# Kernel tuning notes

Measured on AMD Instinct MI355X. Metric: run time of the kernel, lower is better.

## Reference

```python
import jax, jax.numpy as jnp
import numpy as np

INPUT_SZ = 512
HIDDEN_SZ = 512
BATCH = 64
SEQ = 512


def setup_inputs() -> dict:
    key = jax.random.key(0)
    k_x, k_ih, k_hh = jax.random.split(key, 3)
    x = jax.random.normal(k_x, (BATCH, SEQ, INPUT_SZ), dtype=jnp.float32)
    # xavier-uniform style init for 2-D params, zeros for bias (as in init_weights)
    lim_ih = float(np.sqrt(6.0 / (INPUT_SZ + 4 * HIDDEN_SZ)))
    lim_hh = float(np.sqrt(6.0 / (HIDDEN_SZ + 4 * HIDDEN_SZ)))
    weight_ih = jax.random.uniform(k_ih, (INPUT_SZ, 4 * HIDDEN_SZ), jnp.float32, -lim_ih, lim_ih)
    weight_hh = jax.random.uniform(k_hh, (HIDDEN_SZ, 4 * HIDDEN_SZ), jnp.float32, -lim_hh, lim_hh)
    bias = jnp.zeros((4 * HIDDEN_SZ,), jnp.float32)
    h0 = jnp.zeros((1, BATCH, HIDDEN_SZ), jnp.float32)
    c0 = jnp.zeros((1, BATCH, HIDDEN_SZ), jnp.float32)
    return {"x": x, "weight_ih": weight_ih, "weight_hh": weight_hh, "bias": bias, "h0": h0, "c0": c0}


def reference(x, weight_ih, weight_hh, bias, h0, c0):
    HS = weight_hh.shape[0]
    # Precompute input projection for all timesteps: (seq, batch, 4*HS)
    x_proj = jnp.einsum('bsi,ih->sbh', x, weight_ih)

    def step(carry, xp_t):
        h_t, c_t = carry  # (1, b, HS)
        gates = xp_t[None] + h_t @ weight_hh + bias  # (1, b, 4*HS)
        i_t = jax.nn.sigmoid(gates[..., :HS])
        f_t = jax.nn.sigmoid(gates[..., HS:2 * HS])
        g_t = jnp.tanh(gates[..., 2 * HS:3 * HS])
        o_t = jax.nn.sigmoid(gates[..., 3 * HS:])
        c_t = f_t * c_t + i_t * g_t
        h_t = o_t * jnp.tanh(c_t)
        return (h_t, c_t), h_t[0]  # emit (b, HS)

    (h_T, c_T), hs = jax.lax.scan(step, (h0, c0), x_proj)
    hidden_seq = jnp.transpose(hs, (1, 0, 2))  # (batch, seq, HS)
    return hidden_seq, h_T, c_T
```

## Files before the change

### kernel.cpp

```cpp
#include <hip/hip_runtime.h>

#define SEQ   512
#define BATCH 64
#define IS    512
#define HS    512
#define G4    2048

typedef _Float16 half8 __attribute__((ext_vector_type(8)));
typedef _Float16 half4 __attribute__((ext_vector_type(4)));
typedef float floatx4 __attribute__((ext_vector_type(4)));
typedef unsigned long long ull;

__device__ __forceinline__ float sigm(float x) {
    return 1.0f / (1.0f + __expf(-x));
}
__device__ __forceinline__ float tanh_(float x) {
    float e = __expf(-2.0f * fabsf(x));
    float r = (1.0f - e) / (1.0f + e);
    return copysignf(r, x);
}

__global__ void convert_f32_f16(const float* __restrict__ in,
                                _Float16* __restrict__ out, int n4) {
    int i = blockIdx.x * blockDim.x + threadIdx.x;
    if (i < n4) {
        float4 v = ((const float4*)in)[i];
        half4 o = { (_Float16)v.x, (_Float16)v.y, (_Float16)v.z, (_Float16)v.w };
        ((half4*)out)[i] = o;
    }
}

__global__ void transpose_w(const float* __restrict__ in, _Float16* __restrict__ out) {
    __shared__ _Float16 tile[64][72];
    int bk = blockIdx.x & 7;
    int bn = blockIdx.x >> 3;
    int c = threadIdx.x & 63;
    int r4 = threadIdx.x >> 6;
    #pragma unroll
    for (int rr = 0; rr < 16; rr++) {
        int k = rr * 4 + r4;
        tile[k][c] = (_Float16)in[(size_t)(bk * 64 + k) * 2048 + bn * 64 + c];
    }
    __syncthreads();
    #pragma unroll
    for (int rr = 0; rr < 16; rr++) {
        int n = rr * 4 + r4;
        out[(size_t)(bn * 64 + n) * 512 + bk * 64 + c] = tile[c][n];
    }
}

__global__ void __launch_bounds__(256, 2) gemm_xproj(
    const _Float16* __restrict__ A,
    const _Float16* __restrict__ Bt,
    _Float16* __restrict__ xp) {
    __shared__ _Float16 As[4096];
    __shared__ _Float16 Bs[4096];
    const int tid = threadIdx.x;
    const int w = tid >> 6, l = tid & 63, lr = l & 15, q = l >> 4;
    const int bm = blockIdx.x & 255, bn = blockIdx.x >> 8;
    const int row0 = bm * 128, col0 = bn * 128;
    const int wr = (w >> 1) * 64, wc = (w & 1) * 64;

    floatx4 zz = {0.f, 0.f, 0.f, 0.f};
    floatx4 acc[4][4];
    #pragma unroll
    for (int mt = 0; mt < 4; mt++)
        #pragma unroll
        for (int ct = 0; ct < 4; ct++) acc[mt][ct] = zz;

    for (int kt = 0; kt < 16; kt++) {
        __syncthreads();
        #pragma unroll
        for (int rnd = 0; rnd < 2; rnd++) {
            int o = tid * 16 + rnd * 4096;
            int r = o >> 6;
            int ke = (o & 63) >> 1;
            *(half8*)((char*)As + o) = *(const half8*)(A  + (size_t)(row0 + r) * 512 + kt * 32 + ke);
            *(half8*)((char*)Bs + o) = *(const half8*)(Bt + (size_t)(col0 + r) * 512 + kt * 32 + ke);
        }
        __syncthreads();
        half8 af[4], bf[4];
        #pragma unroll
        for (int mt = 0; mt < 4; mt++)
            af[mt] = *(const half8*)(As + (wr + mt * 16 + lr) * 32 + q * 8);
        #pragma unroll
        for (int ct = 0; ct < 4; ct++)
            bf[ct] = *(const half8*)(Bs + (wc + ct * 16 + lr) * 32 + q * 8);
        #pragma unroll
        for (int mt = 0; mt < 4; mt++)
            #pragma unroll
            for (int ct = 0; ct < 4; ct++)
                acc[mt][ct] = __builtin_amdgcn_mfma_f32_16x16x32_f16(af[mt], bf[ct], acc[mt][ct], 0, 0, 0);
    }
    #pragma unroll
    for (int mt = 0; mt < 4; mt++) {
        #pragma unroll
        for (int r = 0; r < 4; r++) {
            int row = row0 + wr + mt * 16 + q * 4 + r;
            int t = row & 511, b = row >> 9;
            #pragma unroll
            for (int ct = 0; ct < 4; ct++) {
                int col = col0 + wc + ct * 16 + lr;
                int hid = col & 511, gate = col >> 9;
                int wgd = (b >> 4) * 32 + (hid >> 4);
                int bl = b & 15, u = hid & 15;
                xp[(size_t)(((t * 128 + wgd) * 16 + bl)) * 64 + u * 4 + gate] =
                    (_Float16)acc[mt][ct][r];
            }
        }
    }
}

__global__ void __launch_bounds__(64, 1) lstm_scan(
    const _Float16* __restrict__ xp,
    const _Float16* __restrict__ wt,
    _Float16* __restrict__ hb,
    const float* __restrict__ bias,
    const float* __restrict__ h0,
    const float* __restrict__ c0,
    float* __restrict__ out,
    int* __restrict__ ep) {
    __shared__ _Float16 wlds[16384];
    __shared__ _Float16 scr[320];
    const int wg = blockIdx.x;
    const int bg = wg >> 5;
    const int hg = wg & 31;
    const int l  = threadIdx.x;
    const int lr = l & 15;
    const int q  = l >> 4;
    const int myhid = hg * 16 + lr;

    for (int idx = l; idx < 2048; idx += 64) {
        int n = idx >> 6, g = idx & 63;
        int gate = n >> 4, u = n & 15;
        half8 v = *(const half8*)(wt + (size_t)(gate * 512 + hg * 16 + u) * 512 + g * 8);
        *(half8*)(wlds + n * 512 + ((g ^ (n & 7)) * 8)) = v;
    }
    half8 wreg[16][2];
    #pragma unroll
    for (int kt = 0; kt < 16; kt++)
        #pragma unroll
        for (int gg = 0; gg < 2; gg++)
            wreg[kt][gg] = *(const half8*)(wt + (size_t)((2 + gg) * 512 + hg * 16 + lr) * 512 + kt * 32 + q * 8);

    {
        int b = l >> 2, u4 = (l & 3) * 4;
        union { _Float16 h[4]; ull u; } pk;
        #pragma unroll
        for (int k2 = 0; k2 < 4; k2++)
            pk.h[k2] = (_Float16)h0[(bg * 16 + b) * 512 + hg * 16 + u4 + k2];
        __hip_atomic_store((ull*)hb + bg * 2048 + b * 128 + hg * 4 + (l & 3), pk.u,
                           __ATOMIC_RELAXED, __HIP_MEMORY_SCOPE_AGENT);
    }

    float bs[4], c[4];
    #pragma unroll
    for (int g4 = 0; g4 < 4; g4++) bs[g4] = bias[g4 * 512 + myhid];
    #pragma unroll
    for (int r = 0; r < 4; r++) c[r] = c0[(bg * 16 + q * 4 + r) * 512 + myhid];

    half4 xv[4];
    #pragma unroll
    for (int r = 0; r < 4; r++)
        xv[r] = *(const half4*)(xp + (((size_t)0 * 128 + wg) * 16 + q * 4 + r) * 64 + lr * 4);

    asm volatile("s_waitcnt vmcnt(0)" ::: "memory");
    if (l == 0)
        __hip_atomic_store(&ep[bg * 32 + hg], 1,
                           __ATOMIC_RELAXED, __HIP_MEMORY_SCOPE_AGENT);

    int* const eline = &ep[bg * 32 + (l & 31)];

    for (int t = 0; t < 512; t++) {
        const int tgt = t + 1;
        while (!__all(__hip_atomic_load(eline, __ATOMIC_RELAXED,
                                        __HIP_MEMORY_SCOPE_AGENT) >= tgt)) { }
        asm volatile("" ::: "memory");
        __builtin_amdgcn_sched_barrier(0);

        const ull* hsrc = (const ull*)hb + (size_t)((t & 1) * 4 + bg) * 2048;
        union HU { ull u[2]; half8 v; } a[16];
        #pragma unroll
        for (int kt = 0; kt < 16; kt++) {
            int idx = lr * 128 + kt * 8 + q * 2;
            a[kt].u[0] = __hip_atomic_load(hsrc + idx,     __ATOMIC_RELAXED, __HIP_MEMORY_SCOPE_AGENT);
            a[kt].u[1] = __hip_atomic_load(hsrc + idx + 1, __ATOMIC_RELAXED, __HIP_MEMORY_SCOPE_AGENT);
        }

        half4 xvn[4];
        {
            int tn = (t + 1) & 511;
            #pragma unroll
            for (int r = 0; r < 4; r++)
                xvn[r] = *(const half4*)(xp + (((size_t)tn * 128 + wg) * 16 + q * 4 + r) * 64 + lr * 4);
        }

        floatx4 zz = {0.f, 0.f, 0.f, 0.f};
        floatx4 acc[4] = {zz, zz, zz, zz};
        floatx4 acc2[4] = {zz, zz, zz, zz};
        #pragma unroll
        for (int kt = 0; kt < 16; kt++) {
            half8 bL[2];
            #pragma unroll
            for (int g4 = 0; g4 < 2; g4++) {
                int n = g4 * 16 + lr;
                bL[g4] = *(const half8*)(wlds + n * 512 + (((kt * 4 + q) ^ (n & 7)) * 8));
            }
            if ((kt & 1) == 0) {
                acc[0] = __builtin_amdgcn_mfma_f32_16x16x32_f16(a[kt].v, bL[0], acc[0], 0, 0, 0);
                acc[1] = __builtin_amdgcn_mfma_f32_16x16x32_f16(a[kt].v, bL[1], acc[1], 0, 0, 0);
                acc[2] = __builtin_amdgcn_mfma_f32_16x16x32_f16(a[kt].v, wreg[kt][0], acc[2], 0, 0, 0);
                acc[3] = __builtin_amdgcn_mfma_f32_16x16x32_f16(a[kt].v, wreg[kt][1], acc[3], 0, 0, 0);
            } else {
                acc2[0] = __builtin_amdgcn_mfma_f32_16x16x32_f16(a[kt].v, bL[0], acc2[0], 0, 0, 0);
                acc2[1] = __builtin_amdgcn_mfma_f32_16x16x32_f16(a[kt].v, bL[1], acc2[1], 0, 0, 0);
                acc2[2] = __builtin_amdgcn_mfma_f32_16x16x32_f16(a[kt].v, wreg[kt][0], acc2[2], 0, 0, 0);
                acc2[3] = __builtin_amdgcn_mfma_f32_16x16x32_f16(a[kt].v, wreg[kt][1], acc2[3], 0, 0, 0);
            }
        }

        float hv[4];
        #pragma unroll
        for (int r = 0; r < 4; r++) {
            float gi = acc[0][r] + acc2[0][r] + (float)xv[r][0] + bs[0];
            float gf = acc[1][r] + acc2[1][r] + (float)xv[r][1] + bs[1];
            float gg = acc[2][r] + acc2[2][r] + (float)xv[r][2] + bs[2];
            float go = acc[3][r] + acc2[3][r] + (float)xv[r][3] + bs[3];
            float i_ = sigm(gi), f_ = sigm(gf), gv = tanh_(gg), o_ = sigm(go);
            c[r] = f_ * c[r] + i_ * gv;
            float h = o_ * tanh_(c[r]);
            hv[r] = h;
            scr[(q * 4 + r) * 20 + lr] = (_Float16)h;
        }
        asm volatile("s_waitcnt lgkmcnt(0)" ::: "memory");
        union { half4 h; ull u; } pk;
        pk.h = *(const half4*)(scr + (l >> 2) * 20 + (l & 3) * 4);

        __hip_atomic_store((ull*)hb + (size_t)(((t + 1) & 1) * 4 + bg) * 2048
                               + (l >> 2) * 128 + hg * 4 + (l & 3), pk.u,
                           __ATOMIC_RELAXED, __HIP_MEMORY_SCOPE_AGENT);
        #pragma unroll
        for (int r = 0; r < 4; r++) {
            int b = bg * 16 + q * 4 + r;
            out[(size_t)b * 262144 + (size_t)t * 512 + myhid] = hv[r];
            if (t == 511) {
                out[16777216 + b * 512 + myhid] = hv[r];
                out[16777216 + 32768 + b * 512 + myhid] = c[r];
            }
        }
        asm volatile("s_waitcnt vmcnt(0)" ::: "memory");
        if (l == 0)
            __hip_atomic_store(&ep[bg * 32 + hg], t + 2,
                               __ATOMIC_RELAXED, __HIP_MEMORY_SCOPE_AGENT);

        #pragma unroll
        for (int r = 0; r < 4; r++) xv[r] = xvn[r];
    }
}

extern "C" void kernel_launch(void* const* d_in, const int* in_sizes, int n_in,
                              void* d_out, int out_size, void* d_ws, size_t ws_size,
                              hipStream_t stream) {
    const float* x    = (const float*)d_in[0];
    const float* wih  = (const float*)d_in[1];
    const float* whh  = (const float*)d_in[2];
    const float* bias = (const float*)d_in[3];
    const float* h0   = (const float*)d_in[4];
    const float* c0   = (const float*)d_in[5];
    float* out = (float*)d_out;

    char* ws = (char*)d_ws;
    _Float16* x16  = (_Float16*)(ws);
    _Float16* wtih = (_Float16*)(ws + 33554432);
    _Float16* wthh = (_Float16*)(ws + 35651584);
    _Float16* xp   = (_Float16*)(ws + 37748736);
    _Float16* hb   = (_Float16*)(ws + 171966464);
    int*      ep   = (int*)(ws + 172097536);

    convert_f32_f16<<<16384, 256, 0, stream>>>(x, x16, BATCH * SEQ * IS / 4);
    transpose_w<<<256, 256, 0, stream>>>(wih, wtih);
    transpose_w<<<256, 256, 0, stream>>>(whh, wthh);
    gemm_xproj<<<4096, 256, 0, stream>>>(x16, wtih, xp);
    hipMemsetAsync(ep, 0, 4096, stream);
    lstm_scan<<<128, 64, 0, stream>>>(xp, wthh, hb, bias, h0, c0, out, ep);
}
```

Baseline: 2.052 ms.

## Replace epoch-flag barrier with poisoned triple-buffered hidden-state exchange

Drops the per-step epoch counter spin and instead triple-buffers the hidden-state exchange, marking not-yet-written slots with an all-ones poison value. Readers speculatively load the next h buffer right after publishing their own slice, then re-poll only if any loaded word is still poison. This removes one global round trip (flag store plus flag poll) from the serial critical path of every timestep. It relies on real fp16 h values never matching the poison bit pattern, and it needs an extra memset of the buffers.

```diff
diff --git a/kernel.cpp b/kernel.cpp
--- a/kernel.cpp
+++ b/kernel.cpp
@@ -118,8 +118,7 @@
     const float* __restrict__ bias,
     const float* __restrict__ h0,
     const float* __restrict__ c0,
-    float* __restrict__ out,
-    int* __restrict__ ep) {
+    float* __restrict__ out) {
     __shared__ _Float16 wlds[16384];
     __shared__ _Float16 scr[320];
     const int wg = blockIdx.x;
@@ -129,6 +128,7 @@
     const int lr = l & 15;
     const int q  = l >> 4;
     const int myhid = hg * 16 + lr;
+    const ull POISON = ~0ull;
 
     for (int idx = l; idx < 2048; idx += 64) {
         int n = idx >> 6, g = idx & 63;
@@ -143,14 +143,19 @@
         for (int gg = 0; gg < 2; gg++)
             wreg[kt][gg] = *(const half8*)(wt + (size_t)((2 + gg) * 512 + hg * 16 + lr) * 512 + kt * 32 + q * 8);
 
+    ull* b0 = (ull*)hb + 0 * 8192 + bg * 2048;
+    ull* b1 = (ull*)hb + 1 * 8192 + bg * 2048;
+    ull* b2 = (ull*)hb + 2 * 8192 + bg * 2048;
+
+    const int punit = (l >> 2) * 128 + hg * 4 + (l & 3);
+
     {
         int b = l >> 2, u4 = (l & 3) * 4;
         union { _Float16 h[4]; ull u; } pk;
         #pragma unroll
         for (int k2 = 0; k2 < 4; k2++)
             pk.h[k2] = (_Float16)h0[(bg * 16 + b) * 512 + hg * 16 + u4 + k2];
-        __hip_atomic_store((ull*)hb + bg * 2048 + b * 128 + hg * 4 + (l & 3), pk.u,
-                           __ATOMIC_RELAXED, __HIP_MEMORY_SCOPE_AGENT);
+        __hip_atomic_store(b0 + punit, pk.u, __ATOMIC_RELAXED, __HIP_MEMORY_SCOPE_AGENT);
     }
 
     float bs[4], c[4];
@@ -159,40 +164,42 @@
     #pragma unroll
     for (int r = 0; r < 4; r++) c[r] = c0[(bg * 16 + q * 4 + r) * 512 + myhid];
 
+    union HU { ull u[2]; half8 v; } a[16];
+    #pragma unroll
+    for (int kt = 0; kt < 16; kt++) {
+        int idx = lr * 128 + kt * 8 + q * 2;
+        a[kt].u[0] = __hip_atomic_load(b0 + idx,     __ATOMIC_RELAXED, __HIP_MEMORY_SCOPE_AGENT);
+        a[kt].u[1] = __hip_atomic_load(b0 + idx + 1, __ATOMIC_RELAXED, __HIP_MEMORY_SCOPE_AGENT);
+    }
     half4 xv[4];
     #pragma unroll
     for (int r = 0; r < 4; r++)
         xv[r] = *(const half4*)(xp + (((size_t)0 * 128 + wg) * 16 + q * 4 + r) * 64 + lr * 4);
 
-    asm volatile("s_waitcnt vmcnt(0)" ::: "memory");
-    if (l == 0)
-        __hip_atomic_store(&ep[bg * 32 + hg], 1,
-                           __ATOMIC_RELAXED, __HIP_MEMORY_SCOPE_AGENT);
-
-    int* const eline = &ep[bg * 32 + (l & 31)];
+    ull* pcur = b0;
+    ull* pnxt = b1;
+    ull* ppoi = b2;
 
     for (int t = 0; t < 512; t++) {
-        const int tgt = t + 1;
-        while (!__all(__hip_atomic_load(eline, __ATOMIC_RELAXED,
-                                        __HIP_MEMORY_SCOPE_AGENT) >= tgt)) { }
-        asm volatile("" ::: "memory");
+        asm volatile("s_waitcnt vmcnt(0)" ::: "memory");
         __builtin_amdgcn_sched_barrier(0);
-
-        const ull* hsrc = (const ull*)hb + (size_t)((t & 1) * 4 + bg) * 2048;
-        union HU { ull u[2]; half8 v; } a[16];
-        #pragma unroll
-        for (int kt = 0; kt < 16; kt++) {
-            int idx = lr * 128 + kt * 8 + q * 2;
-            a[kt].u[0] = __hip_atomic_load(hsrc + idx,     __ATOMIC_RELAXED, __HIP_MEMORY_SCOPE_AGENT);
-            a[kt].u[1] = __hip_atomic_load(hsrc + idx + 1, __ATOMIC_RELAXED, __HIP_MEMORY_SCOPE_AGENT);
-        }
-
-        half4 xvn[4];
-        {
-            int tn = (t + 1) & 511;
-            #pragma unroll
-            for (int r = 0; r < 4; r++)
-                xvn[r] = *(const half4*)(xp + (((size_t)tn * 128 + wg) * 16 + q * 4 + r) * 64 + lr * 4);
+        int stale = 0;
+        #pragma unroll
+        for (int kt = 0; kt < 16; kt++)
+            stale |= (int)(a[kt].u[0] == POISON) | (int)(a[kt].u[1] == POISON);
+        while (__any(stale)) {
+            #pragma unroll
+            for (int kt = 0; kt < 16; kt++) {
+                int idx = lr * 128 + kt * 8 + q * 2;
+                a[kt].u[0] = __hip_atomic_load(pcur + idx,     __ATOMIC_RELAXED, __HIP_MEMORY_SCOPE_AGENT);
+                a[kt].u[1] = __hip_atomic_load(pcur + idx + 1, __ATOMIC_RELAXED, __HIP_MEMORY_SCOPE_AGENT);
+            }
+            asm volatile("s_waitcnt vmcnt(0)" ::: "memory");
+            __builtin_amdgcn_sched_barrier(0);
+            stale = 0;
+            #pragma unroll
+            for (int kt = 0; kt < 16; kt++)
+                stale |= (int)(a[kt].u[0] == POISON) | (int)(a[kt].u[1] == POISON);
         }
 
         floatx4 zz = {0.f, 0.f, 0.f, 0.f};
@@ -233,12 +240,24 @@
             scr[(q * 4 + r) * 20 + lr] = (_Float16)h;
         }
         asm volatile("s_waitcnt lgkmcnt(0)" ::: "memory");
+        __builtin_amdgcn_sched_barrier(0);
         union { half4 h; ull u; } pk;
         pk.h = *(const half4*)(scr + (l >> 2) * 20 + (l & 3) * 4);
 
-        __hip_atomic_store((ull*)hb + (size_t)(((t + 1) & 1) * 4 + bg) * 2048
-                               + (l >> 2) * 128 + hg * 4 + (l & 3), pk.u,
-                           __ATOMIC_RELAXED, __HIP_MEMORY_SCOPE_AGENT);
+        if (t < 511) {
+            __hip_atomic_store(pnxt + punit, pk.u, __ATOMIC_RELAXED, __HIP_MEMORY_SCOPE_AGENT);
+            __hip_atomic_store(ppoi + punit, POISON, __ATOMIC_RELAXED, __HIP_MEMORY_SCOPE_AGENT);
+            #pragma unroll
+            for (int kt = 0; kt < 16; kt++) {
+                int idx = lr * 128 + kt * 8 + q * 2;
+                a[kt].u[0] = __hip_atomic_load(pnxt + idx,     __ATOMIC_RELAXED, __HIP_MEMORY_SCOPE_AGENT);
+                a[kt].u[1] = __hip_atomic_load(pnxt + idx + 1, __ATOMIC_RELAXED, __HIP_MEMORY_SCOPE_AGENT);
+            }
+            #pragma unroll
+            for (int r = 0; r < 4; r++)
+                xv[r] = *(const half4*)(xp + (((size_t)(t + 1) * 128 + wg) * 16 + q * 4 + r) * 64 + lr * 4);
+        }
+
         #pragma unroll
         for (int r = 0; r < 4; r++) {
             int b = bg * 16 + q * 4 + r;
@@ -248,13 +267,8 @@
                 out[16777216 + 32768 + b * 512 + myhid] = c[r];
             }
         }
-        asm volatile("s_waitcnt vmcnt(0)" ::: "memory");
-        if (l == 0)
-            __hip_atomic_store(&ep[bg * 32 + hg], t + 2,
-                               __ATOMIC_RELAXED, __HIP_MEMORY_SCOPE_AGENT);
-
-        #pragma unroll
-        for (int r = 0; r < 4; r++) xv[r] = xvn[r];
+
+        ull* tmp = pcur; pcur = pnxt; pnxt = ppoi; ppoi = tmp;
     }
 }
 
@@ -275,12 +289,11 @@
     _Float16* wthh = (_Float16*)(ws + 35651584);
     _Float16* xp   = (_Float16*)(ws + 37748736);
     _Float16* hb   = (_Float16*)(ws + 171966464);
-    int*      ep   = (int*)(ws + 172097536);
 
     convert_f32_f16<<<16384, 256, 0, stream>>>(x, x16, BATCH * SEQ * IS / 4);
     transpose_w<<<256, 256, 0, stream>>>(wih, wtih);
     transpose_w<<<256, 256, 0, stream>>>(whh, wthh);
     gemm_xproj<<<4096, 256, 0, stream>>>(x16, wtih, xp);
-    hipMemsetAsync(ep, 0, 4096, stream);
-    lstm_scan<<<128, 64, 0, stream>>>(xp, wthh, hb, bias, h0, c0, out, ep);
-}
+    hipMemsetAsync(hb, 0xFF, 196608, stream);
+    lstm_scan<<<128, 64, 0, stream>>>(xp, wthh, hb, bias, h0, c0, out);
+}
```

New measurement: 2.995 ms. 1.46x slower.
